# Kernel optimization log

Measured on AMD Instinct MI355X. Metric: run time of the kernel, lower is better.

## Reference

```python
import jax, jax.numpy as jnp
import numpy as np

B, L, D = 2, 384, 128
N, DHS, DHP = 8, 16, 4  # heads, scalar head dim, point head dim
D_SCALAR = N * DHS          # 128
D_POINT = N * DHP * 3       # 96
D_OUT_IN = D_SCALAR + D * N + D_POINT + N * DHP  # 1280


def setup_inputs() -> dict:
    key = jax.random.key(0)
    ks = jax.random.split(key, 14)
    sc = 0.05
    x = jax.random.normal(ks[0], (B, L, D), dtype=jnp.float32)
    e = jax.random.normal(ks[1], (B, L, L, D), dtype=jnp.float32)
    r = jax.random.normal(ks[2], (B, L, 3, 3), dtype=jnp.float32)
    t = jax.random.normal(ks[3], (B, L, 3), dtype=jnp.float32)
    Wq_s = jax.random.normal(ks[4], (D, D_SCALAR)) * sc
    Wk_s = jax.random.normal(ks[5], (D, D_SCALAR)) * sc
    Wv_s = jax.random.normal(ks[6], (D, D_SCALAR)) * sc
    Wb = jax.random.normal(ks[7], (D, N)) * sc
    Wq_p = jax.random.normal(ks[8], (D, D_POINT)) * sc
    Wk_p = jax.random.normal(ks[9], (D, D_POINT)) * sc
    Wv_p = jax.random.normal(ks[10], (D, D_POINT)) * sc
    gamma = jnp.full((N,), float(np.log(np.exp(1.0) - 1.0)), dtype=jnp.float32)
    Wo = jax.random.normal(ks[11], (D_OUT_IN, D)) * sc
    bo = jnp.zeros((D,), dtype=jnp.float32)
    return {"x": x, "e": e, "r": r, "t": t, "Wq_s": Wq_s, "Wk_s": Wk_s,
            "Wv_s": Wv_s, "Wb": Wb, "Wq_p": Wq_p, "Wk_p": Wk_p,
            "Wv_p": Wv_p, "gamma": gamma, "Wo": Wo, "bo": bo}


def _heads_scalar(y):  # (b,l,n*d) -> (b,n,l,d)
    b, l, _ = y.shape
    return y.reshape(b, l, N, DHS).transpose(0, 2, 1, 3)


def _heads_point(y):  # (b,l,n*p*3) -> (b,n,l,p,3)
    b, l, _ = y.shape
    return y.reshape(b, l, N, DHP, 3).transpose(0, 2, 1, 3, 4)


def reference(x, e, r, t, Wq_s, Wk_s, Wv_s, Wb, Wq_p, Wk_p, Wv_p, gamma, Wo, bo):
    b, l, _ = x.shape
    qs = _heads_scalar(x @ Wq_s)
    ks_ = _heads_scalar(x @ Wk_s)
    vs = _heads_scalar(x @ Wv_s)

    # local points -> global frame: x_row @ r + t (note row-vector convention)
    t_b = t[:, None, :, None, :]  # (b,1,l,1,3)
    qp = jnp.einsum('bnlpk,blkc->bnlpc', _heads_point(x @ Wq_p), r) + t_b
    kp = jnp.einsum('bnlpk,blkc->bnlpc', _heads_point(x @ Wk_p), r) + t_b
    vp = jnp.einsum('bnlpk,blkc->bnlpc', _heads_point(x @ Wv_p), r) + t_b

    logit_scalar = jnp.einsum('bnid,bnjd->bnij', qs, ks_) * (DHS ** -0.5)
    bias_pair = jnp.einsum('bijd,dn->bnij', e, Wb)

    # sum_{p,c} (q_i - k_j)^2 via norm expansion (same math, no O(l^2 p 3) tensor)
    qq = jnp.sum(qp * qp, axis=(-1, -2))  # (b,n,i)
    kk = jnp.sum(kp * kp, axis=(-1, -2))  # (b,n,j)
    cross = jnp.einsum('bnipc,bnjpc->bnij', qp, kp)
    dist2 = qq[..., :, None] + kk[..., None, :] - 2.0 * cross
    logit_point = (-0.5 * 0.25) * gamma[None, :, None, None] * dist2

    logit = (3.0 ** -0.5) * (logit_scalar + bias_pair + logit_point)
    attn = jax.nn.softmax(logit, axis=-1)  # (b,n,i,j)

    out_scalar = jnp.einsum('bnij,bnjd->bnid', attn, vs)
    out_scalar = out_scalar.transpose(0, 2, 1, 3).reshape(b, l, N * DHS)

    out_pair = jnp.einsum('bnij,bijd->bnid', attn, e)
    out_pair = out_pair.transpose(0, 2, 1, 3).reshape(b, l, N * D)

    op = jnp.einsum('bnij,bnjpc->bnipc', attn, vp)
    # inverse transform: (x - t) @ r^T  -> out[c] = sum_k (x-t)[k] * r[c,k]
    op_local = jnp.einsum('bnipk,bick->bnipc', op - t_b, r)
    op_norm = jnp.linalg.norm(op_local, axis=-1)  # (b,n,i,p)

    out_point = op_local.transpose(0, 2, 1, 3, 4).reshape(b, l, N * DHP * 3)
    out_norm = op_norm.transpose(0, 2, 1, 3).reshape(b, l, N * DHP)

    out = jnp.concatenate([out_scalar, out_pair, out_point, out_norm], axis=-1)
    return out @ Wo + bo
```

## Files before the change

### kernel.cpp

```cpp
#include <hip/hip_runtime.h>

#define BB 2
#define LL 384
#define DD 128
#define NH 8

typedef const float* fp32p;

#define AS_G(p) (const __attribute__((address_space(1))) void*)(p)
#define AS_L(p) (__attribute__((address_space(3))) void*)(p)

__global__ __launch_bounds__(128) void k_proj(
    fp32p x, fp32p r, fp32p tvec,
    fp32p Wqs, fp32p Wks, fp32p Wvs,
    fp32p Wqp, fp32p Wkp, fp32p Wvp,
    float* qs, float* ks, float* vs,
    float* qp, float* kp, float* vp)
{
  int bl = blockIdx.x;
  int t = threadIdx.x;
  __shared__ float xs[128];
  __shared__ float yq[96], yk[96], yv[96];
  xs[t] = x[bl*128 + t];
  __syncthreads();
  float aq = 0.f, ak = 0.f, av = 0.f;
  for (int d = 0; d < 128; ++d) {
    float xv = xs[d];
    aq += xv * Wqs[d*128 + t];
    ak += xv * Wks[d*128 + t];
    av += xv * Wvs[d*128 + t];
  }
  int b = bl / LL, l = bl - (bl / LL) * LL;
  int n = t >> 4, dhs = t & 15;
  int rowbase = (b*NH + n)*LL + l;
  qs[rowbase*16 + dhs] = aq;
  ks[rowbase*16 + dhs] = ak;
  vs[rowbase*16 + dhs] = av;
  if (t < 96) {
    float pq = 0.f, pk = 0.f, pv = 0.f;
    for (int d = 0; d < 128; ++d) {
      float xv = xs[d];
      pq += xv * Wqp[d*96 + t];
      pk += xv * Wkp[d*96 + t];
      pv += xv * Wvp[d*96 + t];
    }
    yq[t] = pq; yk[t] = pk; yv[t] = pv;
  }
  __syncthreads();
  if (t < 96) {
    int np = t / 12;
    int rem = t - np*12;
    int p = rem / 3, c = rem - p*3;
    float rr0 = r[(bl*3 + 0)*3 + c];
    float rr1 = r[(bl*3 + 1)*3 + c];
    float rr2 = r[(bl*3 + 2)*3 + c];
    float tt  = tvec[bl*3 + c];
    int base = np*12 + p*3;
    int prow = (b*NH + np)*LL + l;
    qp[prow*12 + p*3 + c] = yq[base]*rr0 + yq[base+1]*rr1 + yq[base+2]*rr2 + tt;
    kp[prow*12 + p*3 + c] = yk[base]*rr0 + yk[base+1]*rr1 + yk[base+2]*rr2 + tt;
    vp[prow*12 + p*3 + c] = yv[base]*rr0 + yv[base+1]*rr1 + yv[base+2]*rr2 + tt;
  }
}

__global__ __launch_bounds__(256) void k_bias(fp32p e, fp32p Wb, float* bias)
{
  int tid = blockIdx.x*256 + threadIdx.x;
  int b = tid / (LL*LL);
  int rem = tid - b*(LL*LL);
  int i = rem / LL, j = rem - (rem / LL)*LL;
  const float4* erow = reinterpret_cast<const float4*>(e) + (size_t)tid * 32;
  float acc[8] = {0,0,0,0,0,0,0,0};
  #pragma unroll
  for (int it = 0; it < 32; ++it) {
    float4 v4 = erow[it];
    float vv[4] = {v4.x, v4.y, v4.z, v4.w};
    #pragma unroll
    for (int k = 0; k < 4; ++k) {
      float v = vv[k];
      #pragma unroll
      for (int nn = 0; nn < 8; ++nn) acc[nn] += v * Wb[(it*4 + k)*8 + nn];
    }
  }
  #pragma unroll
  for (int nn = 0; nn < 8; ++nn)
    bias[(((size_t)(b*NH + nn)*LL + i)*LL) + j] = acc[nn];
}

__global__ __launch_bounds__(256) void k_fused(
    const float* __restrict__ qs, const float* __restrict__ ks,
    const float* __restrict__ vs, const float* __restrict__ qp,
    const float* __restrict__ kp, const float* __restrict__ vp,
    const float* __restrict__ bias, fp32p gamma, fp32p e,
    float* __restrict__ cat, float* __restrict__ opb)
{
  __shared__ float eS[2][32*128];
  __shared__ float lgS[NH*LL];
  __shared__ float sS[NH];

  int bi = blockIdx.x;
  int b = bi / LL, i = bi - (bi / LL)*LL;
  int t = threadIdx.x;
  int n = t >> 5, l32 = t & 31;
  int wbase = t & 192;

  const float4* e4 = reinterpret_cast<const float4*>(e) + (size_t)bi * (LL*DD/4);

  {
    float4* dst = reinterpret_cast<float4*>(eS[0]);
    #pragma unroll
    for (int rd = 0; rd < 4; ++rd)
      __builtin_amdgcn_global_load_lds(AS_G(e4 + rd*256 + t),
                                       AS_L(dst + rd*256 + wbase), 16, 0, 0);
  }

  int rowq = (b*NH + n)*LL + i;
  int rowbase = (b*NH + n)*LL;
  float q[16], qpv[12];
  {
    const float4* q4 = reinterpret_cast<const float4*>(qs + (size_t)rowq*16);
    #pragma unroll
    for (int k2 = 0; k2 < 4; ++k2) { float4 v = q4[k2]; q[4*k2]=v.x; q[4*k2+1]=v.y; q[4*k2+2]=v.z; q[4*k2+3]=v.w; }
    const float4* p4 = reinterpret_cast<const float4*>(qp + (size_t)rowq*12);
    #pragma unroll
    for (int k2 = 0; k2 < 3; ++k2) { float4 v = p4[k2]; qpv[4*k2]=v.x; qpv[4*k2+1]=v.y; qpv[4*k2+2]=v.z; qpv[4*k2+3]=v.w; }
  }
  float qq = 0.f;
  #pragma unroll
  for (int k2 = 0; k2 < 12; ++k2) qq += qpv[k2]*qpv[k2];
  float coef = -0.125f * gamma[n];
  const float* brow = bias + (size_t)rowq*LL;
  for (int jj = 0; jj < 12; ++jj) {
    int j = l32 + jj*32;
    const float4* k4 = reinterpret_cast<const float4*>(ks + (size_t)(rowbase + j)*16);
    float dots = 0.f;
    #pragma unroll
    for (int k2 = 0; k2 < 4; ++k2) {
      float4 v = k4[k2];
      dots += q[4*k2]*v.x + q[4*k2+1]*v.y + q[4*k2+2]*v.z + q[4*k2+3]*v.w;
    }
    const float4* kp4 = reinterpret_cast<const float4*>(kp + (size_t)(rowbase + j)*12);
    float cross = 0.f, kk = 0.f;
    #pragma unroll
    for (int k2 = 0; k2 < 3; ++k2) {
      float4 v = kp4[k2];
      cross += qpv[4*k2]*v.x + qpv[4*k2+1]*v.y + qpv[4*k2+2]*v.z + qpv[4*k2+3]*v.w;
      kk += v.x*v.x + v.y*v.y + v.z*v.z + v.w*v.w;
    }
    lgS[n*LL + j] = 0.57735027f * (0.25f*dots + brow[j] + coef*(qq + kk - 2.f*cross));
  }
  __syncthreads();

  int wv = t >> 6, ln = t & 63;
  for (int nn = wv; nn < 8; nn += 4) {
    float v[6]; float m = -1e30f;
    #pragma unroll
    for (int k2 = 0; k2 < 6; ++k2) { v[k2] = lgS[nn*LL + ln + 64*k2]; m = fmaxf(m, v[k2]); }
    #pragma unroll
    for (int off = 32; off >= 1; off >>= 1) m = fmaxf(m, __shfl_xor(m, off, 64));
    float s = 0.f;
    #pragma unroll
    for (int k2 = 0; k2 < 6; ++k2) { float p = __expf(v[k2] - m); s += p; lgS[nn*LL + ln + 64*k2] = p; }
    #pragma unroll
    for (int off = 32; off >= 1; off >>= 1) s += __shfl_xor(s, off, 64);
    if (ln == 0) sS[nn] = s;
  }
  __syncthreads();

  float4 pacc = {0.f, 0.f, 0.f, 0.f};
  float sacc = 0.f;
  const float* pn = lgS + n*LL;
  const float* vrow0; int vstr;
  if (l32 < 16) { vrow0 = vs + (size_t)rowbase*16 + l32; vstr = 16; }
  else { int comp = (l32 < 28) ? (l32 - 16) : 0; vrow0 = vp + (size_t)rowbase*12 + comp; vstr = 12; }

  for (int tile = 0; tile < 12; ++tile) {
    if (tile < 11) {
      const float4* src = e4 + (tile+1)*1024;
      float4* dst = reinterpret_cast<float4*>(eS[(tile+1)&1]);
      #pragma unroll
      for (int rd = 0; rd < 4; ++rd)
        __builtin_amdgcn_global_load_lds(AS_G(src + rd*256 + t),
                                         AS_L(dst + rd*256 + wbase), 16, 0, 0);
    }
    const float* eT = eS[tile&1];
    const float* pt0 = pn + tile*32;
    const float* vrow = vrow0 + (size_t)tile*32*vstr;
    #pragma unroll 4
    for (int jj = 0; jj < 32; ++jj) {
      float a = pt0[jj];
      float4 ev = *reinterpret_cast<const float4*>(eT + jj*128 + l32*4);
      pacc.x += a*ev.x; pacc.y += a*ev.y; pacc.z += a*ev.z; pacc.w += a*ev.w;
      sacc += a * vrow[(size_t)jj*vstr];
    }
    __syncthreads();
  }

  float inv = 1.f / sS[n];
  float* cbase = cat + (size_t)bi*1280;
  if (l32 < 16)       cbase[n*16 + l32] = sacc * inv;
  else if (l32 < 28)  opb[(size_t)rowq*12 + (l32 - 16)] = sacc * inv;
  float4 pw;
  pw.x = pacc.x*inv; pw.y = pacc.y*inv; pw.z = pacc.z*inv; pw.w = pacc.w*inv;
  *reinterpret_cast<float4*>(cbase + 128 + n*128 + l32*4) = pw;
}

__global__ __launch_bounds__(256) void k_pt(const float* opb, fp32p r, fp32p tvec, float* cat)
{
  int tid = blockIdx.x*256 + threadIdx.x;
  int p = tid & 3;
  int row = tid >> 2;
  int i = row % LL;
  int bn = row / LL;
  int b = bn >> 3, n = bn & 7;
  int bi = b*LL + i;
  float o[3];
  #pragma unroll
  for (int k = 0; k < 3; ++k)
    o[k] = opb[(size_t)row*12 + p*3 + k] - tvec[bi*3 + k];
  float loc[3];
  #pragma unroll
  for (int c = 0; c < 3; ++c) {
    float s = 0.f;
    #pragma unroll
    for (int k = 0; k < 3; ++k) s += o[k] * r[(bi*3 + c)*3 + k];
    loc[c] = s;
  }
  float* dst = cat + (size_t)bi*1280;
  dst[1152 + n*12 + p*3 + 0] = loc[0];
  dst[1152 + n*12 + p*3 + 1] = loc[1];
  dst[1152 + n*12 + p*3 + 2] = loc[2];
  dst[1248 + n*4 + p] = sqrtf(loc[0]*loc[0] + loc[1]*loc[1] + loc[2]*loc[2]);
}

__global__ __launch_bounds__(256) void k_out(const float* cat, fp32p Wo, fp32p bo,
                                             float* out)
{
  __shared__ float catS[2*1280];
  __shared__ float red[2*128];
  int row0 = blockIdx.x*2;
  for (int idx = threadIdx.x; idx < 2*1280; idx += 256)
    catS[idx] = cat[(size_t)row0*1280 + idx];
  __syncthreads();
  int col = threadIdx.x & 127, half = threadIdx.x >> 7;
  float a0 = 0.f, a1 = 0.f;
  int k0 = half*640;
  for (int k = k0; k < k0 + 640; ++k) {
    float w = Wo[k*128 + col];
    a0 += catS[k]        * w;
    a1 += catS[1280 + k] * w;
  }
  if (half) { red[col] = a0; red[128 + col] = a1; }
  __syncthreads();
  if (!half) {
    float bv = bo[col];
    out[(size_t)(row0 + 0)*128 + col] = a0 + red[col]       + bv;
    out[(size_t)(row0 + 1)*128 + col] = a1 + red[128 + col] + bv;
  }
}

extern "C" void kernel_launch(void* const* d_in, const int* in_sizes, int n_in,
                              void* d_out, int out_size, void* d_ws, size_t ws_size,
                              hipStream_t stream)
{
  fp32p x    = (fp32p)d_in[0];
  fp32p e    = (fp32p)d_in[1];
  fp32p r    = (fp32p)d_in[2];
  fp32p tv   = (fp32p)d_in[3];
  fp32p Wqs  = (fp32p)d_in[4];
  fp32p Wks  = (fp32p)d_in[5];
  fp32p Wvs  = (fp32p)d_in[6];
  fp32p Wb   = (fp32p)d_in[7];
  fp32p Wqp  = (fp32p)d_in[8];
  fp32p Wkp  = (fp32p)d_in[9];
  fp32p Wvp  = (fp32p)d_in[10];
  fp32p gam  = (fp32p)d_in[11];
  fp32p Wo   = (fp32p)d_in[12];
  fp32p bo   = (fp32p)d_in[13];
  float* out = (float*)d_out;

  float* qs   = (float*)d_ws;
  float* ks   = qs + 98304;
  float* vs   = ks + 98304;
  float* qp   = vs + 98304;
  float* kp   = qp + 73728;
  float* vp   = kp + 73728;
  float* bias = vp + 73728;
  float* opb  = bias + 2359296;
  float* cat  = opb + 73728;

  k_proj<<<768, 128, 0, stream>>>(x, r, tv, Wqs, Wks, Wvs, Wqp, Wkp, Wvp,
                                  qs, ks, vs, qp, kp, vp);
  k_bias<<<1152, 256, 0, stream>>>(e, Wb, bias);
  k_fused<<<768, 256, 0, stream>>>(qs, ks, vs, qp, kp, vp, bias, gam, e, cat, opb);
  k_pt<<<96, 256, 0, stream>>>(opb, r, tv, cat);
  k_out<<<384, 256, 0, stream>>>(cat, Wo, bo, out);
}
```

Baseline: 370.5 us.

## Fuse point-inverse-transform into output GEMM, halve e tile, unroll loops

After: 372.4 us. Within noise of the previous version (+0.5%).

```diff
diff --git a/kernel.cpp b/kernel.cpp
--- a/kernel.cpp
+++ b/kernel.cpp
@@ -24,6 +24,7 @@
   xs[t] = x[bl*128 + t];
   __syncthreads();
   float aq = 0.f, ak = 0.f, av = 0.f;
+  #pragma unroll 8
   for (int d = 0; d < 128; ++d) {
     float xv = xs[d];
     aq += xv * Wqs[d*128 + t];
@@ -38,6 +39,7 @@
   vs[rowbase*16 + dhs] = av;
   if (t < 96) {
     float pq = 0.f, pk = 0.f, pv = 0.f;
+    #pragma unroll 8
     for (int d = 0; d < 128; ++d) {
       float xv = xs[d];
       pq += xv * Wqp[d*96 + t];
@@ -94,7 +96,7 @@
     const float* __restrict__ bias, fp32p gamma, fp32p e,
     float* __restrict__ cat, float* __restrict__ opb)
 {
-  __shared__ float eS[2][32*128];
+  __shared__ float eS[2][16*128];
   __shared__ float lgS[NH*LL];
   __shared__ float sS[NH];
 
@@ -109,7 +111,7 @@
   {
     float4* dst = reinterpret_cast<float4*>(eS[0]);
     #pragma unroll
-    for (int rd = 0; rd < 4; ++rd)
+    for (int rd = 0; rd < 2; ++rd)
       __builtin_amdgcn_global_load_lds(AS_G(e4 + rd*256 + t),
                                        AS_L(dst + rd*256 + wbase), 16, 0, 0);
   }
@@ -174,20 +176,20 @@
   if (l32 < 16) { vrow0 = vs + (size_t)rowbase*16 + l32; vstr = 16; }
   else { int comp = (l32 < 28) ? (l32 - 16) : 0; vrow0 = vp + (size_t)rowbase*12 + comp; vstr = 12; }
 
-  for (int tile = 0; tile < 12; ++tile) {
-    if (tile < 11) {
-      const float4* src = e4 + (tile+1)*1024;
+  for (int tile = 0; tile < 24; ++tile) {
+    if (tile < 23) {
+      const float4* src = e4 + (tile+1)*512;
       float4* dst = reinterpret_cast<float4*>(eS[(tile+1)&1]);
       #pragma unroll
-      for (int rd = 0; rd < 4; ++rd)
+      for (int rd = 0; rd < 2; ++rd)
         __builtin_amdgcn_global_load_lds(AS_G(src + rd*256 + t),
                                          AS_L(dst + rd*256 + wbase), 16, 0, 0);
     }
     const float* eT = eS[tile&1];
-    const float* pt0 = pn + tile*32;
-    const float* vrow = vrow0 + (size_t)tile*32*vstr;
+    const float* pt0 = pn + tile*16;
+    const float* vrow = vrow0 + (size_t)tile*16*vstr;
     #pragma unroll 4
-    for (int jj = 0; jj < 32; ++jj) {
+    for (int jj = 0; jj < 16; ++jj) {
       float a = pt0[jj];
       float4 ev = *reinterpret_cast<const float4*>(eT + jj*128 + l32*4);
       pacc.x += a*ev.x; pacc.y += a*ev.y; pacc.z += a*ev.z; pacc.w += a*ev.w;
@@ -205,46 +207,42 @@
   *reinterpret_cast<float4*>(cbase + 128 + n*128 + l32*4) = pw;
 }
 
-__global__ __launch_bounds__(256) void k_pt(const float* opb, fp32p r, fp32p tvec, float* cat)
-{
-  int tid = blockIdx.x*256 + threadIdx.x;
-  int p = tid & 3;
-  int row = tid >> 2;
-  int i = row % LL;
-  int bn = row / LL;
-  int b = bn >> 3, n = bn & 7;
-  int bi = b*LL + i;
-  float o[3];
-  #pragma unroll
-  for (int k = 0; k < 3; ++k)
-    o[k] = opb[(size_t)row*12 + p*3 + k] - tvec[bi*3 + k];
-  float loc[3];
-  #pragma unroll
-  for (int c = 0; c < 3; ++c) {
-    float s = 0.f;
-    #pragma unroll
-    for (int k = 0; k < 3; ++k) s += o[k] * r[(bi*3 + c)*3 + k];
-    loc[c] = s;
-  }
-  float* dst = cat + (size_t)bi*1280;
-  dst[1152 + n*12 + p*3 + 0] = loc[0];
-  dst[1152 + n*12 + p*3 + 1] = loc[1];
-  dst[1152 + n*12 + p*3 + 2] = loc[2];
-  dst[1248 + n*4 + p] = sqrtf(loc[0]*loc[0] + loc[1]*loc[1] + loc[2]*loc[2]);
-}
-
-__global__ __launch_bounds__(256) void k_out(const float* cat, fp32p Wo, fp32p bo,
-                                             float* out)
+__global__ __launch_bounds__(256) void k_tail(
+    const float* cat, const float* opb, fp32p rvec, fp32p tvec,
+    fp32p Wo, fp32p bo, float* out)
 {
   __shared__ float catS[2*1280];
   __shared__ float red[2*128];
   int row0 = blockIdx.x*2;
-  for (int idx = threadIdx.x; idx < 2*1280; idx += 256)
-    catS[idx] = cat[(size_t)row0*1280 + idx];
-  __syncthreads();
-  int col = threadIdx.x & 127, half = threadIdx.x >> 7;
+  int t = threadIdx.x;
+  for (int idx = t; idx < 2304; idx += 256) {
+    int rr = idx / 1152, off = idx - rr*1152;
+    catS[rr*1280 + off] = cat[(size_t)(row0 + rr)*1280 + off];
+  }
+  if (t < 192) {
+    int rr = t / 96;
+    int dim = t - rr*96;
+    int n = dim / 12, pk = dim - n*12, p = pk / 3, c = pk - p*3;
+    int rg = row0 + rr;
+    int b = rg / LL, i = rg - b*LL;
+    const float* oprow = opb + (size_t)((b*NH + n)*LL + i) * 12;
+    float o0 = oprow[p*3 + 0] - tvec[rg*3 + 0];
+    float o1 = oprow[p*3 + 1] - tvec[rg*3 + 1];
+    float o2 = oprow[p*3 + 2] - tvec[rg*3 + 2];
+    const float* rb = rvec + (size_t)rg*9;
+    float loc = o0*rb[c*3 + 0] + o1*rb[c*3 + 1] + o2*rb[c*3 + 2];
+    catS[rr*1280 + 1152 + n*12 + p*3 + c] = loc;
+    if (c == 0) {
+      float l1 = o0*rb[3] + o1*rb[4] + o2*rb[5];
+      float l2 = o0*rb[6] + o1*rb[7] + o2*rb[8];
+      catS[rr*1280 + 1248 + n*4 + p] = sqrtf(loc*loc + l1*l1 + l2*l2);
+    }
+  }
+  __syncthreads();
+  int col = t & 127, half = t >> 7;
   float a0 = 0.f, a1 = 0.f;
   int k0 = half*640;
+  #pragma unroll 8
   for (int k = k0; k < k0 + 640; ++k) {
     float w = Wo[k*128 + col];
     a0 += catS[k]        * w;
@@ -293,6 +291,5 @@
                                   qs, ks, vs, qp, kp, vp);
   k_bias<<<1152, 256, 0, stream>>>(e, Wb, bias);
   k_fused<<<768, 256, 0, stream>>>(qs, ks, vs, qp, kp, vp, bias, gam, e, cat, opb);
-  k_pt<<<96, 256, 0, stream>>>(opb, r, tv, cat);
-  k_out<<<384, 256, 0, stream>>>(cat, Wo, bo, out);
-}
+  k_tail<<<384, 256, 0, stream>>>(cat, opb, r, tv, Wo, bo, out);
+}
```
